# Performance work log

Hardware: AMD Instinct MI355X
Metric: run time of the kernel (lower is better)

Reference implementation:

```python
import jax, jax.numpy as jnp
import numpy as np

N_ENT = 100000
K = 64
D = 500            # emb_dim (complex half-dim); entity embedding is 2*D
R = 237            # num_relations
ATTN = 128
B = 1024
ETA_MAX = 0.5


def setup_inputs() -> dict:
    key = jax.random.key(0)
    ks = jax.random.split(key, 12)
    anchor_ids = jax.random.randint(ks[0], (B,), 0, N_ENT)
    nbr_ent = jax.random.randint(ks[1], (N_ENT, K), 0, N_ENT)
    nbr_rel = jax.random.randint(ks[2], (N_ENT, K), 0, R)
    nbr_dir = jax.random.randint(ks[3], (N_ENT, K), 0, 2).astype(bool)
    nbr_mask = jax.random.randint(ks[4], (N_ENT, K), 0, 2).astype(bool)
    freq = jax.random.uniform(ks[5], (N_ENT,), dtype=jnp.float32) * 1000.0
    entity_embedding = jax.random.normal(ks[6], (N_ENT, 2 * D), dtype=jnp.float32) * 0.1
    # relation phases; get_relation_reim -> (cos(phase), sin(phase))
    rel_phase = jax.random.uniform(ks[7], (R, D), dtype=jnp.float32, minval=-np.pi, maxval=np.pi)
    a_param = jnp.ones((D,), dtype=jnp.float32)
    eta_raw = jnp.float32(-6.0)
    w_raw = jnp.float32(1.0)
    b = jnp.float32(0.0)
    Wq = jax.random.normal(ks[8], (ATTN, 2 * D), dtype=jnp.float32) * 0.01
    Wk = jax.random.normal(ks[9], (ATTN, 2 * D), dtype=jnp.float32) * 0.01
    rel_bias = jax.random.normal(ks[10], (R, 1), dtype=jnp.float32) * 0.01
    dir_bias = jax.random.normal(ks[11], (2, 1), dtype=jnp.float32) * 0.01
    return dict(anchor_ids=anchor_ids, nbr_ent=nbr_ent, nbr_rel=nbr_rel,
                nbr_dir=nbr_dir, nbr_mask=nbr_mask, freq=freq,
                entity_embedding=entity_embedding, rel_phase=rel_phase,
                a_param=a_param, eta_raw=eta_raw, w_raw=w_raw, b=b,
                Wq=Wq, Wk=Wk, rel_bias=rel_bias, dir_bias=dir_bias)


def reference(anchor_ids, nbr_ent, nbr_rel, nbr_dir, nbr_mask, freq,
              entity_embedding, rel_phase, a_param, eta_raw, w_raw, b,
              Wq, Wk, rel_bias, dir_bias):
    # gather per-anchor neighbor tables: [B, K]
    a_ent = nbr_ent[anchor_ids]
    a_rel = nbr_rel[anchor_ids]
    a_dir = nbr_dir[anchor_ids]
    a_msk = nbr_mask[anchor_ids]

    # neighbor entity embeddings [B, K, 2D] -> complex halves [B, K, D]
    e_j = entity_embedding[a_ent]
    re_j, im_j = jnp.split(e_j, 2, axis=-1)

    # RotatE relation rotation (conjugate when dir==True)
    phase = rel_phase[a_rel]                      # [B, K, D]
    re_r = jnp.cos(phase)
    im_r = jnp.sin(phase)
    im_sel = jnp.where(a_dir[..., None], -im_r, im_r)
    re_msg = re_j * re_r - im_j * im_sel
    im_msg = re_j * im_sel + im_j * re_r
    hat = jnp.concatenate([re_msg, im_msg], axis=-1)  # [B, K, 2D]

    e_i = entity_embedding[anchor_ids]            # [B, 2D]

    # small QK attention with relation/direction bias
    q = e_i @ Wq.T                                # [B, A]
    k = hat @ Wk.T                                # [B, K, A]
    scale = max(ATTN ** 0.5, 1e-6)
    logits = jnp.einsum('ba,bka->bk', q, k) / scale
    dir_id = a_dir.astype(jnp.int32)
    logits = logits + rel_bias[a_rel][..., 0] + dir_bias[dir_id][..., 0]
    logits = jnp.where(a_msk, logits, -10000.0)

    has_nbr = jnp.any(a_msk, axis=1)              # [B]
    logits = jnp.where(has_nbr[:, None], logits, 0.0)
    attn = jax.nn.softmax(logits, axis=1)
    attn = jnp.where(has_nbr[:, None], attn, 0.0)

    delta = jnp.einsum('bk,bkd->bd', attn, hat)   # [B, 2D]
    delta = jnp.where(has_nbr[:, None], delta, e_i)

    # frequency-gated interpolation
    logf = jnp.log1p(freq[anchor_ids])
    w = jax.nn.softplus(w_raw)
    eta = ETA_MAX * jax.nn.sigmoid(eta_raw + w * (-logf) + b)
    eta = eta * has_nbr.astype(eta.dtype)

    re_d, im_d = jnp.split(delta, 2, axis=-1)
    re_d = a_param * re_d
    im_d = a_param * im_d
    re_i, im_i = jnp.split(e_i, 2, axis=-1)
    re_out = re_i + eta[:, None] * (re_d - re_i)
    im_out = im_i + eta[:, None] * (im_d - im_i)
    return jnp.concatenate([re_out, im_out], axis=-1)
```

## Files before the change

kernel.cpp:

```cpp
#include <hip/hip_runtime.h>
#include <math.h>

#define N_ENT 100000
#define KNBR 64
#define DHALF 500
#define TWO_D 1000
#define ATTN_DIM 128
#define NREL 237
#define ETA_MAX 0.5f

__global__ __launch_bounds__(256) void build_trig(
    const float* __restrict__ P, float* __restrict__ CS)
{
    int idx = blockIdx.x * 256 + threadIdx.x;
    if (idx < NREL * DHALF) {
        float s, c;
        sincosf(P[idx], &s, &c);
        CS[2 * idx]     = c;
        CS[2 * idx + 1] = s;
    }
}

__global__ __launch_bounds__(256) void precompute_m(
    const int* __restrict__ anchor_ids,
    const float* __restrict__ E,
    const float* __restrict__ Wq,
    const float* __restrict__ Wk,
    float* __restrict__ M, int B)
{
    __shared__ float e_lds[4][TWO_D];
    __shared__ float qp[2][4][ATTN_DIM];
    __shared__ float q_lds[4][ATTN_DIM];
    const int t  = threadIdx.x;
    const int b0 = blockIdx.x * 4;

    for (int j = 0; j < 4; ++j) {
        int bb = b0 + j;
        int row = (bb < B) ? anchor_ids[bb] : 0;
        if (t < 250) {
            float4 v = ((const float4*)(E + (size_t)row * TWO_D))[t];
            ((float4*)&e_lds[j][0])[t] = v;
        }
    }
    __syncthreads();

    {
        const int a = t & 127;
        const int h = t >> 7;
        float acc[4] = {0.f, 0.f, 0.f, 0.f};
        const float* wrow = Wq + (size_t)a * TWO_D + h * DHALF;
        const int base = h * DHALF;
        for (int d = 0; d < DHALF; ++d) {
            float w = wrow[d];
            int dd = base + d;
#pragma unroll
            for (int j = 0; j < 4; ++j) acc[j] += w * e_lds[j][dd];
        }
#pragma unroll
        for (int j = 0; j < 4; ++j) qp[h][j][a] = acc[j];
    }
    __syncthreads();
    for (int idx = t; idx < 4 * ATTN_DIM; idx += 256)
        ((float*)q_lds)[idx] = ((float*)qp)[idx] + ((float*)qp)[4 * ATTN_DIM + idx];
    __syncthreads();

    const float inv_scale = 0.0883883476483184f;
    float acc2[4][4];
#pragma unroll
    for (int c = 0; c < 4; ++c)
#pragma unroll
        for (int j = 0; j < 4; ++j) acc2[c][j] = 0.f;

    for (int a = 0; a < ATTN_DIM; ++a) {
        const float* wkrow = Wk + (size_t)a * TWO_D;
        float wk[4];
#pragma unroll
        for (int c = 0; c < 4; ++c) {
            int d = t + 256 * c;
            wk[c] = (d < TWO_D) ? wkrow[d] : 0.f;
        }
#pragma unroll
        for (int j = 0; j < 4; ++j) {
            float qv = q_lds[j][a];
#pragma unroll
            for (int c = 0; c < 4; ++c) acc2[c][j] += qv * wk[c];
        }
    }
#pragma unroll
    for (int c = 0; c < 4; ++c) {
        int d = t + 256 * c;
        if (d < TWO_D) {
#pragma unroll
            for (int j = 0; j < 4; ++j) {
                int bb = b0 + j;
                if (bb < B) M[(size_t)bb * TWO_D + d] = acc2[c][j] * inv_scale;
            }
        }
    }
}

__global__ __launch_bounds__(256, 4) void refine(
    const int* __restrict__ anchor_ids,
    const int* __restrict__ nbr_ent,
    const int* __restrict__ nbr_rel,
    const int* __restrict__ nbr_dir,
    const int* __restrict__ nbr_mask,
    const float* __restrict__ freq,
    const float* __restrict__ E,
    const float* __restrict__ CS,
    const float* __restrict__ a_param,
    const float* __restrict__ eta_raw_p,
    const float* __restrict__ w_raw_p,
    const float* __restrict__ b_p,
    const float* __restrict__ rel_bias,
    const float* __restrict__ dir_bias,
    const float* __restrict__ M,
    float* __restrict__ out)
{
    __shared__ float accm[4][TWO_D];
    __shared__ float sum_s[4];
    __shared__ int ent_s[KNBR], rel_s[KNBR], dir_s[KNBR], list_s[KNBR];
    __shared__ int cnt_s;

    const int t = threadIdx.x;
    const int bid = blockIdx.x;
    const int anchor = anchor_ids[bid];
    const int lane = t & 63;
    const int wid = t >> 6;
    const int l1 = (lane < 61) ? lane : 60;

    if (t < KNBR) {
        size_t off = (size_t)anchor * KNBR + t;
        int e = nbr_ent[off];
        int r = nbr_rel[off];
        int d = nbr_dir[off];
        int m = nbr_mask[off];
        ent_s[t] = e; rel_s[t] = r; dir_s[t] = d;
        unsigned long long bal = __ballot(m != 0);
        if (m) list_s[__popcll(bal & ((1ull << t) - 1))] = t;
        if (t == 0) cnt_s = __popcll(bal);
    }

    const float4* Mr = (const float4*)(M + (size_t)bid * TWO_D);
    float4 mre0 = Mr[lane];
    float4 mim0 = Mr[125 + lane];
    float4 mre1 = Mr[64 + l1];
    float4 mim1 = Mr[189 + l1];
    if (lane >= 61) {
        mre1 = make_float4(0.f, 0.f, 0.f, 0.f);
        mim1 = make_float4(0.f, 0.f, 0.f, 0.f);
    }
    float mreA[8] = {mre0.x, mre0.y, mre0.z, mre0.w, mre1.x, mre1.y, mre1.z, mre1.w};
    float mimA[8] = {mim0.x, mim0.y, mim0.z, mim0.w, mim1.x, mim1.y, mim1.z, mim1.w};

    float accre[8], accim[8];
#pragma unroll
    for (int q = 0; q < 8; ++q) { accre[q] = 0.f; accim[q] = 0.f; }
    float wsum = 0.f;
    const float db0 = dir_bias[0];
    const float db1 = dir_bias[1];

    __syncthreads();
    const int n = cnt_s;

    struct NB {
        float4 re0, im0, re1, im1;
        float4 csA, csB, csC, csD;
        float bias, sgn;
    };
    NB A, Bq;

    auto load_nb = [&](NB& nb, int slot) {
        int k = list_s[slot];
        int df = dir_s[k];
        const float4* er = (const float4*)(E + (size_t)ent_s[k] * TWO_D);
        const float4* cr = (const float4*)(CS + (size_t)rel_s[k] * TWO_D);
        nb.re0 = er[lane];          nb.im0 = er[125 + lane];
        nb.re1 = er[64 + l1];       nb.im1 = er[189 + l1];
        nb.csA = cr[2 * lane];      nb.csB = cr[2 * lane + 1];
        nb.csC = cr[128 + 2 * l1];  nb.csD = cr[129 + 2 * l1];
        nb.bias = rel_bias[rel_s[k]] + (df ? db1 : db0);
        nb.sgn = df ? -1.f : 1.f;
    };

    auto compute_nb = [&](const NB& nb) {
        float re_[8] = {nb.re0.x, nb.re0.y, nb.re0.z, nb.re0.w,
                        nb.re1.x, nb.re1.y, nb.re1.z, nb.re1.w};
        float im_[8] = {nb.im0.x, nb.im0.y, nb.im0.z, nb.im0.w,
                        nb.im1.x, nb.im1.y, nb.im1.z, nb.im1.w};
        float cc[8]  = {nb.csA.x, nb.csA.z, nb.csB.x, nb.csB.z,
                        nb.csC.x, nb.csC.z, nb.csD.x, nb.csD.z};
        float ssv[8] = {nb.csA.y, nb.csA.w, nb.csB.y, nb.csB.w,
                        nb.csC.y, nb.csC.w, nb.csD.y, nb.csD.w};
        float hre[8], him[8];
        float dot = 0.f;
#pragma unroll
        for (int q = 0; q < 8; ++q) {
            float sv = ssv[q] * nb.sgn;
            hre[q] = re_[q] * cc[q] - im_[q] * sv;
            him[q] = re_[q] * sv + im_[q] * cc[q];
            dot += mreA[q] * hre[q] + mimA[q] * him[q];
        }
        dot += __shfl_xor(dot, 32);
        dot += __shfl_xor(dot, 16);
        dot += __shfl_xor(dot, 8);
        dot += __shfl_xor(dot, 4);
        dot += __shfl_xor(dot, 2);
        dot += __shfl_xor(dot, 1);
        float p = __expf(dot + nb.bias);
        wsum += p;
#pragma unroll
        for (int q = 0; q < 8; ++q) {
            accre[q] += p * hre[q];
            accim[q] += p * him[q];
        }
    };

    {
        int i = wid;
        bool haveA = (i < n);
        if (haveA) load_nb(A, i);
        while (haveA) {
            int iB = i + 4;
            bool haveB = (iB < n);
            if (haveB) load_nb(Bq, iB);
            compute_nb(A);
            if (!haveB) break;
            int iA = iB + 4;
            haveA = (iA < n);
            if (haveA) load_nb(A, iA);
            compute_nb(Bq);
            i = iA;
        }
    }

    if (lane == 0) sum_s[wid] = wsum;
    {
        float4* arow = (float4*)&accm[wid][0];
        arow[lane]       = make_float4(accre[0], accre[1], accre[2], accre[3]);
        arow[125 + lane] = make_float4(accim[0], accim[1], accim[2], accim[3]);
        if (lane < 61) {
            arow[64 + lane]  = make_float4(accre[4], accre[5], accre[6], accre[7]);
            arow[189 + lane] = make_float4(accim[4], accim[5], accim[6], accim[7]);
        }
    }
    __syncthreads();

    const float S = sum_s[0] + sum_s[1] + sum_s[2] + sum_s[3];
    const float invS = (S > 0.f) ? 1.f / S : 0.f;
    float eta = 0.f;
    if (S > 0.f) {
        float logf_ = log1pf(freq[anchor]);
        float wv = log1pf(__expf(w_raw_p[0]));
        float x = eta_raw_p[0] - wv * logf_ + b_p[0];
        eta = ETA_MAX / (1.f + __expf(-x));
    }

    if (t < 250) {
        const float4* r0 = (const float4*)&accm[0][0];
        const float4* r1 = (const float4*)&accm[1][0];
        const float4* r2 = (const float4*)&accm[2][0];
        const float4* r3 = (const float4*)&accm[3][0];
        float4 a0 = r0[t], a1 = r1[t], a2 = r2[t], a3 = r3[t];
        float4 delta;
        delta.x = (a0.x + a1.x + a2.x + a3.x) * invS;
        delta.y = (a0.y + a1.y + a2.y + a3.y) * invS;
        delta.z = (a0.z + a1.z + a2.z + a3.z) * invS;
        delta.w = (a0.w + a1.w + a2.w + a3.w) * invS;
        const float4* A4 = (const float4*)a_param;
        float4 ap = (t < 125) ? A4[t] : A4[t - 125];
        float4 ei = ((const float4*)(E + (size_t)anchor * TWO_D))[t];
        float4 o;
        o.x = ei.x + eta * (ap.x * delta.x - ei.x);
        o.y = ei.y + eta * (ap.y * delta.y - ei.y);
        o.z = ei.z + eta * (ap.z * delta.z - ei.z);
        o.w = ei.w + eta * (ap.w * delta.w - ei.w);
        ((float4*)(out + (size_t)bid * TWO_D))[t] = o;
    }
}

extern "C" void kernel_launch(void* const* d_in, const int* in_sizes, int n_in,
                              void* d_out, int out_size, void* d_ws, size_t ws_size,
                              hipStream_t stream)
{
    const int*   anchor_ids = (const int*)d_in[0];
    const int*   nbr_ent    = (const int*)d_in[1];
    const int*   nbr_rel    = (const int*)d_in[2];
    const int*   nbr_dir    = (const int*)d_in[3];
    const int*   nbr_mask   = (const int*)d_in[4];
    const float* freq       = (const float*)d_in[5];
    const float* E          = (const float*)d_in[6];
    const float* P          = (const float*)d_in[7];
    const float* a_param    = (const float*)d_in[8];
    const float* eta_raw    = (const float*)d_in[9];
    const float* w_raw      = (const float*)d_in[10];
    const float* b_scalar   = (const float*)d_in[11];
    const float* Wq         = (const float*)d_in[12];
    const float* Wk         = (const float*)d_in[13];
    const float* rel_bias   = (const float*)d_in[14];
    const float* dir_bias   = (const float*)d_in[15];
    float* out = (float*)d_out;

    const int B = in_sizes[0];
    float* M  = (float*)d_ws;
    float* CS = M + (size_t)B * TWO_D;

    build_trig<<<(NREL * DHALF + 255) / 256, 256, 0, stream>>>(P, CS);
    precompute_m<<<(B + 3) / 4, 256, 0, stream>>>(anchor_ids, E, Wq, Wk, M, B);
    refine<<<B, 256, 0, stream>>>(anchor_ids, nbr_ent, nbr_rel, nbr_dir, nbr_mask,
                                  freq, E, CS, a_param, eta_raw, w_raw, b_scalar,
                                  rel_bias, dir_bias, M, out);
}
```

Baseline: 626.2 us.

## Fuse trig table build into precompute kernel and simplify neighbor pipeline

Merges the sincos table kernel into the precompute_m launch as extra blocks, removing one kernel launch. The Wq projection loop is vectorised with float4 loads. In the refine kernel, neighbor data and bias are compacted into shared memory at load time, dropping the indirection through a list. The double-buffered A/B neighbor structs are replaced by a single register set, with the next load issued before the shuffle reduction. This lowers register pressure but leaves less prefetch distance to hide gather latency.

```diff
diff --git a/kernel.cpp b/kernel.cpp
--- a/kernel.cpp
+++ b/kernel.cpp
@@ -9,29 +9,31 @@
 #define NREL 237
 #define ETA_MAX 0.5f
 
-__global__ __launch_bounds__(256) void build_trig(
-    const float* __restrict__ P, float* __restrict__ CS)
-{
-    int idx = blockIdx.x * 256 + threadIdx.x;
-    if (idx < NREL * DHALF) {
-        float s, c;
-        sincosf(P[idx], &s, &c);
-        CS[2 * idx]     = c;
-        CS[2 * idx + 1] = s;
-    }
-}
-
 __global__ __launch_bounds__(256) void precompute_m(
     const int* __restrict__ anchor_ids,
     const float* __restrict__ E,
     const float* __restrict__ Wq,
     const float* __restrict__ Wk,
-    float* __restrict__ M, int B)
+    const float* __restrict__ P,
+    float* __restrict__ CS,
+    float* __restrict__ M, int B, int nM)
 {
+    const int t = threadIdx.x;
+
+    if ((int)blockIdx.x >= nM) {
+        int idx = ((int)blockIdx.x - nM) * 256 + t;
+        if (idx < NREL * DHALF) {
+            float s, c;
+            sincosf(P[idx], &s, &c);
+            CS[2 * idx]     = c;
+            CS[2 * idx + 1] = s;
+        }
+        return;
+    }
+
     __shared__ float e_lds[4][TWO_D];
     __shared__ float qp[2][4][ATTN_DIM];
     __shared__ float q_lds[4][ATTN_DIM];
-    const int t  = threadIdx.x;
     const int b0 = blockIdx.x * 4;
 
     for (int j = 0; j < 4; ++j) {
@@ -48,13 +50,18 @@
         const int a = t & 127;
         const int h = t >> 7;
         float acc[4] = {0.f, 0.f, 0.f, 0.f};
-        const float* wrow = Wq + (size_t)a * TWO_D + h * DHALF;
-        const int base = h * DHALF;
-        for (int d = 0; d < DHALF; ++d) {
-            float w = wrow[d];
-            int dd = base + d;
-#pragma unroll
-            for (int j = 0; j < 4; ++j) acc[j] += w * e_lds[j][dd];
+        const float4* wrow4 = (const float4*)(Wq + (size_t)a * TWO_D + h * DHALF);
+        const float4* e0 = (const float4*)&e_lds[0][h * DHALF];
+        const float4* e1 = (const float4*)&e_lds[1][h * DHALF];
+        const float4* e2 = (const float4*)&e_lds[2][h * DHALF];
+        const float4* e3 = (const float4*)&e_lds[3][h * DHALF];
+        for (int d4 = 0; d4 < DHALF / 4; ++d4) {
+            float4 w = wrow4[d4];
+            float4 v;
+            v = e0[d4]; acc[0] += w.x*v.x + w.y*v.y + w.z*v.z + w.w*v.w;
+            v = e1[d4]; acc[1] += w.x*v.x + w.y*v.y + w.z*v.z + w.w*v.w;
+            v = e2[d4]; acc[2] += w.x*v.x + w.y*v.y + w.z*v.z + w.w*v.w;
+            v = e3[d4]; acc[3] += w.x*v.x + w.y*v.y + w.z*v.z + w.w*v.w;
         }
 #pragma unroll
         for (int j = 0; j < 4; ++j) qp[h][j][a] = acc[j];
@@ -119,8 +126,11 @@
 {
     __shared__ float accm[4][TWO_D];
     __shared__ float sum_s[4];
-    __shared__ int ent_s[KNBR], rel_s[KNBR], dir_s[KNBR], list_s[KNBR];
-    __shared__ int cnt_s;
+    __shared__ int   ent_c[KNBR];
+    __shared__ int   rel_c[KNBR];
+    __shared__ int   dir_c[KNBR];
+    __shared__ float bias_c[KNBR];
+    __shared__ int   cnt_s;
 
     const int t = threadIdx.x;
     const int bid = blockIdx.x;
@@ -135,9 +145,14 @@
         int r = nbr_rel[off];
         int d = nbr_dir[off];
         int m = nbr_mask[off];
-        ent_s[t] = e; rel_s[t] = r; dir_s[t] = d;
         unsigned long long bal = __ballot(m != 0);
-        if (m) list_s[__popcll(bal & ((1ull << t) - 1))] = t;
+        if (m) {
+            int j = __popcll(bal & ((1ull << t) - 1));
+            ent_c[j] = e;
+            rel_c[j] = r;
+            dir_c[j] = d;
+            bias_c[j] = rel_bias[r] + dir_bias[d];
+        }
         if (t == 0) cnt_s = __popcll(bal);
     }
 
@@ -150,87 +165,69 @@
         mre1 = make_float4(0.f, 0.f, 0.f, 0.f);
         mim1 = make_float4(0.f, 0.f, 0.f, 0.f);
     }
-    float mreA[8] = {mre0.x, mre0.y, mre0.z, mre0.w, mre1.x, mre1.y, mre1.z, mre1.w};
-    float mimA[8] = {mim0.x, mim0.y, mim0.z, mim0.w, mim1.x, mim1.y, mim1.z, mim1.w};
+    const float mreA[8] = {mre0.x, mre0.y, mre0.z, mre0.w, mre1.x, mre1.y, mre1.z, mre1.w};
+    const float mimA[8] = {mim0.x, mim0.y, mim0.z, mim0.w, mim1.x, mim1.y, mim1.z, mim1.w};
 
     float accre[8], accim[8];
 #pragma unroll
     for (int q = 0; q < 8; ++q) { accre[q] = 0.f; accim[q] = 0.f; }
     float wsum = 0.f;
-    const float db0 = dir_bias[0];
-    const float db1 = dir_bias[1];
 
     __syncthreads();
     const int n = cnt_s;
 
-    struct NB {
-        float4 re0, im0, re1, im1;
-        float4 csA, csB, csC, csD;
-        float bias, sgn;
+    float4 re0, im0, re1, im1, cA, cB, cC, cD;
+    float bias = 0.f, sgn = 1.f;
+
+    auto load_nb = [&](int slot) {
+        int df = dir_c[slot];
+        const float4* er = (const float4*)(E + (size_t)ent_c[slot] * TWO_D);
+        const float4* cr = (const float4*)(CS + (size_t)rel_c[slot] * TWO_D);
+        bias = bias_c[slot];
+        sgn = df ? -1.f : 1.f;
+        re0 = er[lane];          im0 = er[125 + lane];
+        re1 = er[64 + l1];       im1 = er[189 + l1];
+        cA = cr[2 * lane];       cB = cr[2 * lane + 1];
+        cC = cr[128 + 2 * l1];   cD = cr[129 + 2 * l1];
     };
-    NB A, Bq;
-
-    auto load_nb = [&](NB& nb, int slot) {
-        int k = list_s[slot];
-        int df = dir_s[k];
-        const float4* er = (const float4*)(E + (size_t)ent_s[k] * TWO_D);
-        const float4* cr = (const float4*)(CS + (size_t)rel_s[k] * TWO_D);
-        nb.re0 = er[lane];          nb.im0 = er[125 + lane];
-        nb.re1 = er[64 + l1];       nb.im1 = er[189 + l1];
-        nb.csA = cr[2 * lane];      nb.csB = cr[2 * lane + 1];
-        nb.csC = cr[128 + 2 * l1];  nb.csD = cr[129 + 2 * l1];
-        nb.bias = rel_bias[rel_s[k]] + (df ? db1 : db0);
-        nb.sgn = df ? -1.f : 1.f;
-    };
-
-    auto compute_nb = [&](const NB& nb) {
-        float re_[8] = {nb.re0.x, nb.re0.y, nb.re0.z, nb.re0.w,
-                        nb.re1.x, nb.re1.y, nb.re1.z, nb.re1.w};
-        float im_[8] = {nb.im0.x, nb.im0.y, nb.im0.z, nb.im0.w,
-                        nb.im1.x, nb.im1.y, nb.im1.z, nb.im1.w};
-        float cc[8]  = {nb.csA.x, nb.csA.z, nb.csB.x, nb.csB.z,
-                        nb.csC.x, nb.csC.z, nb.csD.x, nb.csD.z};
-        float ssv[8] = {nb.csA.y, nb.csA.w, nb.csB.y, nb.csB.w,
-                        nb.csC.y, nb.csC.w, nb.csD.y, nb.csD.w};
+
+    int i = wid;
+    bool have = (i < n);
+    if (have) load_nb(i);
+    while (have) {
+        float re_[8] = {re0.x, re0.y, re0.z, re0.w, re1.x, re1.y, re1.z, re1.w};
+        float im_[8] = {im0.x, im0.y, im0.z, im0.w, im1.x, im1.y, im1.z, im1.w};
+        float cc[8]  = {cA.x, cA.z, cB.x, cB.z, cC.x, cC.z, cD.x, cD.z};
+        float ssv[8] = {cA.y, cA.w, cB.y, cB.w, cC.y, cC.w, cD.y, cD.w};
         float hre[8], him[8];
         float dot = 0.f;
 #pragma unroll
         for (int q = 0; q < 8; ++q) {
-            float sv = ssv[q] * nb.sgn;
+            float sv = ssv[q] * sgn;
             hre[q] = re_[q] * cc[q] - im_[q] * sv;
             him[q] = re_[q] * sv + im_[q] * cc[q];
             dot += mreA[q] * hre[q] + mimA[q] * him[q];
         }
+        const float biasC = bias;
+
+        int inext = i + 4;
+        have = (inext < n);
+        if (have) load_nb(inext);
+        i = inext;
+
         dot += __shfl_xor(dot, 32);
         dot += __shfl_xor(dot, 16);
         dot += __shfl_xor(dot, 8);
         dot += __shfl_xor(dot, 4);
         dot += __shfl_xor(dot, 2);
         dot += __shfl_xor(dot, 1);
-        float p = __expf(dot + nb.bias);
+
+        float p = __expf(dot + biasC);
         wsum += p;
 #pragma unroll
         for (int q = 0; q < 8; ++q) {
             accre[q] += p * hre[q];
             accim[q] += p * him[q];
-        }
-    };
-
-    {
-        int i = wid;
-        bool haveA = (i < n);
-        if (haveA) load_nb(A, i);
-        while (haveA) {
-            int iB = i + 4;
-            bool haveB = (iB < n);
-            if (haveB) load_nb(Bq, iB);
-            compute_nb(A);
-            if (!haveB) break;
-            int iA = iB + 4;
-            haveA = (iA < n);
-            if (haveA) load_nb(A, iA);
-            compute_nb(Bq);
-            i = iA;
         }
     }
 
@@ -305,8 +302,9 @@
     float* M  = (float*)d_ws;
     float* CS = M + (size_t)B * TWO_D;
 
-    build_trig<<<(NREL * DHALF + 255) / 256, 256, 0, stream>>>(P, CS);
-    precompute_m<<<(B + 3) / 4, 256, 0, stream>>>(anchor_ids, E, Wq, Wk, M, B);
+    const int nM = (B + 3) / 4;
+    const int nT = (NREL * DHALF + 255) / 256;
+    precompute_m<<<nM + nT, 256, 0, stream>>>(anchor_ids, E, Wq, Wk, P, CS, M, B, nM);
     refine<<<B, 256, 0, stream>>>(anchor_ids, nbr_ent, nbr_rel, nbr_dir, nbr_mask,
                                   freq, E, CS, a_param, eta_raw, w_raw, b_scalar,
                                   rel_bias, dir_bias, M, out);
```

After: 609.8 us. 1.03x faster.
